# Optimization experiments

Hardware: AMD Instinct MI355X
Metric: run time of the kernel (lower is better)

## Reference

```python
import jax, jax.numpy as jnp
import numpy as np
import math

B = 200        # graphs
NPG = 512      # nodes per graph
EPG = 8192     # edges per graph (avg degree 16)
E = B * EPG
FIN = 11
H = 128


def setup_inputs() -> dict:
    key = jax.random.key(0)
    ks = jax.random.split(key, 16)
    g = jnp.arange(E, dtype=jnp.int32) // EPG  # graph id per edge
    edge_src = g * NPG + jax.random.randint(ks[0], (E,), 0, NPG, dtype=jnp.int32)
    edge_dst = g * NPG + jax.random.randint(ks[1], (E,), 0, NPG, dtype=jnp.int32)
    x = jax.random.normal(ks[2], (B * NPG, FIN), dtype=jnp.float32)

    def w(k, shape):
        return jax.random.normal(k, shape, dtype=jnp.float32) * 0.1

    return dict(
        x=x, edge_src=edge_src, edge_dst=edge_dst,
        num_graphs=B, nodes_per_graph=NPG,
        Wrel1=w(ks[3], (H, FIN)), Wroot1=w(ks[4], (H, FIN)), b1=jnp.zeros((H,), jnp.float32), pw1=w(ks[5], (H,)),
        Wrel2=w(ks[6], (H, H)), Wroot2=w(ks[7], (H, H)), b2=jnp.zeros((H,), jnp.float32), pw2=w(ks[8], (H,)),
        Wrel3=w(ks[9], (H, H)), Wroot3=w(ks[10], (H, H)), b3=jnp.zeros((H,), jnp.float32), pw3=w(ks[11], (H,)),
        Wl1=w(ks[12], (512, 256)), bl1=jnp.zeros((512,), jnp.float32),
        Wl2=w(ks[13], (64, 512)), bl2=jnp.zeros((64,), jnp.float32),
        Wl3=w(ks[14], (1, 64)), bl3=jnp.zeros((1,), jnp.float32),
    )


def graph_conv(x, src, dst, emask, Wrel, Wroot, b):
    # PyG GraphConv (aggr='add'): lin_rel(sum_j x_j) + lin_root(x)
    msg = x[src] * emask[:, None]                    # [E, F] gather + edge mask
    agg = jax.ops.segment_sum(msg, dst, num_segments=x.shape[0])
    return agg @ Wrel.T + b + x @ Wroot.T


def topk_pool(x, src, dst, emask, w, ratio, B):
    # PyG TopKPooling: score = tanh((x . w)/||w||), keep top ceil(ratio*N) per graph
    N = x.shape[0] // B
    k = int(math.ceil(ratio * N))
    score = jnp.tanh((x @ w) / jnp.linalg.norm(w))   # [B*N]
    _, idx = jax.lax.top_k(score.reshape(B, N), k)   # local indices per graph
    perm = (idx + (jnp.arange(B, dtype=idx.dtype) * N)[:, None]).reshape(-1)  # [B*k]
    xk = x[perm] * score[perm][:, None]
    # old node id -> new node id (or -1 if dropped); reindex edges, mask invalid
    newid = jnp.full((B * N,), -1, dtype=jnp.int32).at[perm].set(jnp.arange(B * k, dtype=jnp.int32))
    ns, nd = newid[src], newid[dst]
    keep = emask * (ns >= 0) * (nd >= 0)
    return xk, jnp.maximum(ns, 0), jnp.maximum(nd, 0), keep.astype(x.dtype)


def readout(x, B):
    # cat([global_max_pool, global_mean_pool]); uniform graph sizes -> reshape
    xr = x.reshape(B, -1, x.shape[-1])
    return jnp.concatenate([xr.max(axis=1), xr.mean(axis=1)], axis=-1)


def reference(x, edge_src, edge_dst, num_graphs, nodes_per_graph,
              Wrel1, Wroot1, b1, pw1, Wrel2, Wroot2, b2, pw2,
              Wrel3, Wroot3, b3, pw3, Wl1, bl1, Wl2, bl2, Wl3, bl3):
    Bg = num_graphs
    src, dst = edge_src, edge_dst
    emask = jnp.ones(src.shape, x.dtype)
    h = jax.nn.relu(graph_conv(x, src, dst, emask, Wrel1, Wroot1, b1))
    h, src, dst, emask = topk_pool(h, src, dst, emask, pw1, 0.5, Bg)
    x1 = readout(h, Bg)
    h = jax.nn.relu(graph_conv(h, src, dst, emask, Wrel2, Wroot2, b2))
    h, src, dst, emask = topk_pool(h, src, dst, emask, pw2, 0.8, Bg)
    x2 = readout(h, Bg)
    h = jax.nn.relu(graph_conv(h, src, dst, emask, Wrel3, Wroot3, b3))
    h, src, dst, emask = topk_pool(h, src, dst, emask, pw3, 0.8, Bg)
    x3 = readout(h, Bg)
    z = x1 + x2 + x3
    z = jax.nn.relu(z @ Wl1.T + bl1)   # dropout p=0.7 is identity in eval mode
    z = jax.nn.relu(z @ Wl2.T + bl2)
    return z @ Wl3.T + bl3             # [B, 1]
```

## Files before the change

kernel.cpp:

```cpp
#include <hip/hip_runtime.h>
#include <math.h>

#define BG   200
#define NPGc 512
#define EPGc 8192
#define NE   (BG*EPGc)
#define N0   (BG*NPGc)
#define FINc 11
#define Hc   128
#define K1c  256
#define K2c  205
#define K3c  164
#define N1   (BG*K1c)
#define N2   (BG*K2c)
#define N3   (BG*K3c)

typedef float f32x4 __attribute__((ext_vector_type(4)));
typedef short s16x8 __attribute__((ext_vector_type(8)));

#define PL ((size_t)N1*Hc)
#define PA ((size_t)N0*32)

__device__ inline unsigned short bf16_rne(float v){
  unsigned u = __float_as_uint(v);
  unsigned r = u + 0x7FFFu + ((u >> 16) & 1u);
  return (unsigned short)(r >> 16);
}
__device__ inline float bf16_f32(unsigned short h){
  return __uint_as_float(((unsigned)h) << 16);
}
__device__ inline void split3(float v, unsigned short& r0, unsigned short& r1,
                              unsigned short& r2){
  r0 = bf16_rne(v); float v1 = v - bf16_f32(r0);
  r1 = bf16_rne(v1); float v2 = v1 - bf16_f32(r1);
  r2 = bf16_rne(v2);
}

__device__ inline size_t flIdx(int row, int k){
  return ((size_t)(row >> 4))*2048 + (size_t)(k >> 3)*128
       + (size_t)(row & 15)*8 + (size_t)(k & 7);
}
__device__ inline size_t flIdx32(int row, int k){
  return ((size_t)(row >> 4))*512 + (size_t)(k >> 3)*128
       + (size_t)(row & 15)*8 + (size_t)(k & 7);
}

__launch_bounds__(512)
__global__ void k_front(const int* __restrict__ esrc, const int* __restrict__ edst,
                        const float* __restrict__ x,
                        const float* __restrict__ Wrel1, const float* __restrict__ Wroot1,
                        const float* __restrict__ Wrel2, const float* __restrict__ Wroot2,
                        const float* __restrict__ Wrel3, const float* __restrict__ Wroot3,
                        const float* __restrict__ Wl1, const float* __restrict__ Wl2,
                        const float* __restrict__ pw1, const float* __restrict__ pw2,
                        const float* __restrict__ pw3,
                        int* __restrict__ deg, int* __restrict__ rowptr,
                        int* __restrict__ csr, float* __restrict__ xp,
                        float* __restrict__ Wl1T, float* __restrict__ Wl2T,
                        unsigned short* __restrict__ Wsp, unsigned short* __restrict__ W1S,
                        float* __restrict__ z, float* __restrict__ norms){
  int b = blockIdx.x, t = threadIdx.x;
  if (b < BG){
    __shared__ int ed[EPGc];
    __shared__ int cnt[NPGc];
    __shared__ int sc[NPGc];
    int g = b;
    cnt[t] = 0;
    __syncthreads();
    int gb = g*EPGc;
    for (int i=t; i<EPGc; i+=512){
      int dl = edst[gb+i] & (NPGc-1);
      ed[i] = dl;
      atomicAdd(&cnt[dl], 1);
    }
    __syncthreads();
    int d = cnt[t];
    sc[t] = d;
    __syncthreads();
    for (int o=1;o<NPGc;o<<=1){
      int v = (t>=o) ? sc[t-o] : 0;
      __syncthreads();
      sc[t] += v;
      __syncthreads();
    }
    deg[g*NPGc+t]    = d;
    rowptr[g*NPGc+t] = gb + sc[t] - d;
    cnt[t] = sc[t] - d;
    __syncthreads();
    for (int i=t; i<EPGc; i+=512){
      int p = atomicAdd(&cnt[ed[i]], 1);
      csr[gb+p] = esrc[gb+i];
    }
  } else if (b < 456){
    int idx = (b-200)*512 + t;
    if (idx < 256*512){
      int f = idx >> 9, tt = idx & 511;
      Wl1T[idx] = Wl1[tt*256 + f];
    }
    if (idx < 512*64){
      int f = idx >> 6, tt = idx & 63;
      Wl2T[idx] = Wl2[tt*512 + f];
    }
    if (idx < 65536){
      int L = idx >> 15, p = (idx >> 14) & 1, ck = idx & 16383;
      int c = ck >> 7, k = ck & 127;
      const float* W = L ? (p ? Wroot3 : Wrel3) : (p ? Wroot2 : Wrel2);
      unsigned short r0, r1, r2;
      split3(W[c*128 + k], r0, r1, r2);
      unsigned short* base = Wsp + (size_t)((L*2+p)*3)*16384;
      size_t fl = flIdx(c, k);
      base[fl]          = r0;
      base[16384 + fl]  = r1;
      base[32768 + fl]  = r2;
    }
    if (idx < 4096){
      int c = idx >> 5, k = idx & 31;
      float v = (k < 11) ? Wrel1[c*11 + k] : (k < 22 ? Wroot1[c*11 + (k-11)] : 0.f);
      unsigned short r0, r1, r2;
      split3(v, r0, r1, r2);
      size_t fl = flIdx32(c, k);
      W1S[fl]        = r0;
      W1S[4096 + fl] = r1;
      W1S[8192 + fl] = r2;
    }
    if (idx < BG*256) z[idx] = 0.f;
    if (b == 455){
      int w = t >> 6, lane = t & 63;
      if (w < 3){
        const float* pw = (w==0) ? pw1 : (w==1 ? pw2 : pw3);
        float v0 = pw[lane], v1 = pw[64+lane];
        float ss = v0*v0 + v1*v1;
        for (int o=32;o>0;o>>=1) ss += __shfl_xor(ss, o);
        if (lane == 0) norms[w] = sqrtf(ss);
      }
    }
  } else {
    int idx = (b-456)*512 + t;
    int n = idx >> 4, f = idx & 15;
    xp[idx] = (f < FINc) ? x[n*FINc + f] : 0.f;
  }
}

__launch_bounds__(256, 8)
__global__ void k_agg1s(const float* __restrict__ xp, const int* __restrict__ csr,
                        const int* __restrict__ rowptr, const int* __restrict__ deg,
                        unsigned short* __restrict__ AS){
  int bid = (int)((blockIdx.x & 7)*3200 + (blockIdx.x >> 3));
  int d = bid*4 + (threadIdx.x >> 6);
  if (d >= N0) return;
  int lane = threadIdx.x & 63;
  int slot = lane >> 4, f = lane & 15;
  int rs = rowptr[d], dg = deg[d];
  float a0 = 0.f, a1 = 0.f, a2 = 0.f, a3 = 0.f;
  for (int base=0; base<dg; base+=64){
    int e = base + lane;
    int s = 0;
    if (e < dg) s = csr[rs+e];
    int cnt = min(64, dg-base);
    int sv[16];
    #pragma unroll
    for (int u=0; u<16; u++) sv[u] = __shfl(s, u*4 + slot);
    #pragma unroll
    for (int u=0; u<16; u++){
      int ei = u*4 + slot;
      float v = 0.f;
      if (ei < cnt) v = xp[(sv[u] << 4) + f];
      if      ((u & 3) == 0) a0 += v;
      else if ((u & 3) == 1) a1 += v;
      else if ((u & 3) == 2) a2 += v;
      else                   a3 += v;
    }
  }
  a0 = (a0 + a1) + (a2 + a3);
  a0 += __shfl_xor(a0, 16);
  a0 += __shfl_xor(a0, 32);
  int k0 = 2*lane, k1 = k0 + 1;
  float s0 = __shfl(a0, k0 & 15);
  float s1 = __shfl(a0, k1 & 15);
  if (lane < 16){
    float v0 = (k0 < 11) ? s0 : ((k0 < 22) ? xp[(d<<4) + k0 - 11] : 0.f);
    float v1 = (k1 < 11) ? s1 : ((k1 < 22) ? xp[(d<<4) + k1 - 11] : 0.f);
    unsigned short a_0,a_1,a_2,b_0,b_1,b_2;
    split3(v0, a_0, a_1, a_2);
    split3(v1, b_0, b_1, b_2);
    size_t fl = flIdx32(d, k0);
    *(unsigned*)&AS[fl]        = (unsigned)a_0 | ((unsigned)b_0 << 16);
    *(unsigned*)&AS[PA + fl]   = (unsigned)a_1 | ((unsigned)b_1 << 16);
    *(unsigned*)&AS[2*PA + fl] = (unsigned)a_2 | ((unsigned)b_2 << 16);
  }
}

__launch_bounds__(256)
__global__ void k_conv1m(const unsigned short* __restrict__ AS,
                         const unsigned short* __restrict__ W1S,
                         const float* __restrict__ bias, const float* __restrict__ pw,
                         const float* __restrict__ norm_p,
                         float* __restrict__ hout, float* __restrict__ score, int M){
  __shared__ float scds[64][2];
  int tid = threadIdx.x;
  int w = tid >> 6, l = tid & 63;
  int wm = w >> 1, wn = w & 1;
  int lr = l & 15, lk = l >> 4;
  int m0 = blockIdx.x * 64;

  f32x4 acc[2][4];
  #pragma unroll
  for (int mi=0;mi<2;mi++)
    #pragma unroll
    for (int ni=0;ni<4;ni++) acc[mi][ni] = (f32x4){0.f,0.f,0.f,0.f};

  s16x8 af[3][2], bf[3][4];
  #pragma unroll
  for (int mi=0; mi<2; mi++){
    int tile = (m0 + wm*32 + mi*16) >> 4;
    size_t idx = (size_t)tile*512 + (size_t)lk*128 + (size_t)lr*8;
    af[0][mi] = *(const s16x8*)&AS[idx];
    af[1][mi] = *(const s16x8*)&AS[PA + idx];
    af[2][mi] = *(const s16x8*)&AS[2*PA + idx];
  }
  #pragma unroll
  for (int ni=0; ni<4; ni++){
    int ct = wn*4 + ni;
    size_t idx = (size_t)ct*512 + (size_t)lk*128 + (size_t)lr*8;
    bf[0][ni] = *(const s16x8*)&W1S[idx];
    bf[1][ni] = *(const s16x8*)&W1S[4096 + idx];
    bf[2][ni] = *(const s16x8*)&W1S[8192 + idx];
  }
  #define TRM(sa,sb) \
    _Pragma("unroll") \
    for (int ni=0; ni<4; ni++){ \
      _Pragma("unroll") \
      for (int mi=0; mi<2; mi++){ \
        acc[mi][ni] = __builtin_amdgcn_mfma_f32_16x16x32_bf16(af[sa][mi], bf[sb][ni], acc[mi][ni], 0,0,0); \
      } \
    }
  TRM(0,0) TRM(0,1) TRM(1,0) TRM(1,1) TRM(0,2) TRM(2,0)
  #undef TRM

  float nrm = *norm_p;
  float pwv[4], biasv[4];
  #pragma unroll
  for (int ni=0;ni<4;ni++){
    int col = wn*64 + ni*16 + lr;
    pwv[ni] = pw[col]; biasv[ni] = bias[col];
  }
  #pragma unroll
  for (int mi=0; mi<2; mi++){
    #pragma unroll
    for (int reg=0; reg<4; reg++){
      int rl = wm*32 + mi*16 + lk*4 + reg;
      int row = m0 + rl;
      float hv[4]; float sc = 0.f;
      #pragma unroll
      for (int ni=0; ni<4; ni++){
        hv[ni] = fmaxf(acc[mi][ni][reg] + biasv[ni], 0.f);
        sc += hv[ni]*pwv[ni];
      }
      if (row < M){
        #pragma unroll
        for (int ni=0; ni<4; ni++)
          hout[(size_t)row*Hc + wn*64 + ni*16 + lr] = hv[ni];
      }
      sc += __shfl_xor(sc,1); sc += __shfl_xor(sc,2);
      sc += __shfl_xor(sc,4); sc += __shfl_xor(sc,8);
      if (lr == 0) scds[rl][wn] = sc;
    }
  }
  __syncthreads();
  if (tid < 64){
    int row = m0 + tid;
    if (row < M) score[row] = tanhf((scds[tid][0] + scds[tid][1]) / nrm);
  }
}

template<int N, int K, int NP2, bool DOSPLIT, bool DOMLP>
__launch_bounds__(1024, 4)
__global__ void k_topg(const float* __restrict__ score, const float* __restrict__ h,
                       int* __restrict__ newid, int* __restrict__ perm,
                       const int* __restrict__ map1In, int* __restrict__ map2Out,
                       const int* __restrict__ origPrev, int* __restrict__ origOut,
                       float* __restrict__ hp, unsigned short* __restrict__ hpS,
                       float* __restrict__ z,
                       const float* __restrict__ Wl1T, const float* __restrict__ bl1,
                       const float* __restrict__ Wl2T, const float* __restrict__ bl2,
                       const float* __restrict__ Wl3, const float* __restrict__ bl3,
                       float* __restrict__ out){
  __shared__ float sv[NP2];
  __shared__ int   si[NP2];
  __shared__ int   nid[N];
  __shared__ float2 smx2[16][64];
  __shared__ float2 ssm2[16][64];
  __shared__ float zfin[256];
  __shared__ float u1[512];
  int g = blockIdx.x, t = threadIdx.x;

  float v = -INFINITY; int ix = t;
  if (t < NP2 && t < N) v = score[g*N + t];

  for (int k=2;k<=NP2;k<<=1){
    for (int j=k>>1;j>0;j>>=1){
      if (j >= 64){
        if (t < NP2){ sv[t] = v; si[t] = ix; }
        __syncthreads();
        if (t < NP2){
          int p = t ^ j;
          float vp = sv[p]; int ip = si[p];
          bool pre = (v > vp) || (v == vp && ix < ip);
          bool up = ((t & k) == 0);
          bool lower = ((t & j) == 0);
          bool keep = lower ? (pre == up) : (pre != up);
          if (!keep){ v = vp; ix = ip; }
        }
        __syncthreads();
      } else {
        if (t < NP2){
          float vp = __shfl_xor(v, j);
          int   ip = __shfl_xor(ix, j);
          bool pre = (v > vp) || (v == vp && ix < ip);
          bool up = ((t & k) == 0);
          bool lower = ((t & j) == 0);
          bool keep = lower ? (pre == up) : (pre != up);
          if (!keep){ v = vp; ix = ip; }
        }
      }
    }
  }
  if (t < NP2){ sv[t] = v; si[t] = ix; }
  __syncthreads();

  if (t < N) nid[si[t]] = (t < K) ? t : -1;
  __syncthreads();
  if (t < N) newid[g*N + t] = (nid[t] >= 0) ? g*K + nid[t] : -1;
  if (t < K){
    int old = si[t];
    perm[g*K + t] = g*N + old;
    if (origOut) origOut[g*K + t] = origPrev[g*N + old];
  }
  if (map2Out){
    for (int o = t; o < NPGc; o += 1024){
      int m = map1In[g*NPGc + o];
      int r = (m >= 0) ? nid[m - g*N] : -1;
      map2Out[g*NPGc + o] = (r >= 0) ? g*K + r : -1;
    }
  }
  __syncthreads();

  constexpr int NB = (K + 15) / 16;
  int rg = t >> 6, j2 = t & 63;
  float2 vv[NB];
  #pragma unroll
  for (int i=0; i<NB; i++){
    int r = rg + 16*i;
    float2 val = make_float2(0.f, 0.f);
    if (r < K){
      int old = si[r];
      val = *(const float2*)&h[(size_t)(g*N + old)*Hc + 2*j2];
      float sc = sv[r];
      val.x *= sc; val.y *= sc;
    }
    vv[i] = val;
  }
  float mx = -INFINITY, my = -INFINITY, sx = 0.f, sy = 0.f;
  #pragma unroll
  for (int i=0; i<NB; i++){
    int r = rg + 16*i;
    if (r < K){
      int m = g*K + r;
      if (hp) *(float2*)&hp[(size_t)m*Hc + 2*j2] = vv[i];
      if constexpr (DOSPLIT){
        unsigned short a0,a1,a2,b0,b1,b2;
        split3(vv[i].x, a0, a1, a2);
        split3(vv[i].y, b0, b1, b2);
        size_t fl = flIdx(m, 2*j2);
        *(unsigned*)&hpS[fl]        = (unsigned)a0 | ((unsigned)b0 << 16);
        *(unsigned*)&hpS[PL + fl]   = (unsigned)a1 | ((unsigned)b1 << 16);
        *(unsigned*)&hpS[2*PL + fl] = (unsigned)a2 | ((unsigned)b2 << 16);
      }
      mx = fmaxf(mx, vv[i].x); my = fmaxf(my, vv[i].y);
      sx += vv[i].x; sy += vv[i].y;
    }
  }
  smx2[rg][j2] = make_float2(mx, my);
  ssm2[rg][j2] = make_float2(sx, sy);
  __syncthreads();
  if (t < 64){
    float2 M = smx2[0][t], S = ssm2[0][t];
    #pragma unroll
    for (int u=1; u<16; u++){
      float2 m2 = smx2[u][t], s2 = ssm2[u][t];
      M.x = fmaxf(M.x, m2.x); M.y = fmaxf(M.y, m2.y);
      S.x += s2.x; S.y += s2.y;
    }
    int c0 = 2*t, c1 = 2*t + 1;
    if constexpr (DOMLP){
      zfin[c0]       = z[g*256 + c0]       + M.x;
      zfin[c1]       = z[g*256 + c1]       + M.y;
      zfin[128 + c0] = z[g*256 + 128 + c0] + S.x / (float)K;
      zfin[128 + c1] = z[g*256 + 128 + c1] + S.y / (float)K;
    } else {
      z[g*256 + c0]       += M.x;
      z[g*256 + c1]       += M.y;
      z[g*256 + 128 + c0] += S.x / (float)K;
      z[g*256 + 128 + c1] += S.y / (float)K;
    }
  }
  if constexpr (DOMLP){
    __syncthreads();
    if (t < 512){
      float acc = bl1[t];
      #pragma unroll 8
      for (int f=0; f<256; f++) acc = fmaf(zfin[f], Wl1T[f*512 + t], acc);
      u1[t] = fmaxf(acc, 0.f);
    }
    __syncthreads();
    if (t < 64){
      float acc = bl2[t];
      #pragma unroll 8
      for (int f=0; f<512; f++) acc = fmaf(u1[f], Wl2T[f*64 + t], acc);
      float vy = fmaxf(acc, 0.f) * Wl3[t];
      for (int o=32;o>0;o>>=1) vy += __shfl_xor(vy, o);
      if (t == 0) out[g] = vy + bl3[0];
    }
  }
}

__launch_bounds__(256, 4)
__global__ void k_aggHs(const int* __restrict__ orig, const int* __restrict__ map,
                        const float* __restrict__ hp,
                        const int* __restrict__ csr, const int* __restrict__ rowptr,
                        const int* __restrict__ deg, unsigned short* __restrict__ aggS,
                        int M){
  int cpx = gridDim.x >> 3;
  int bid = (int)((blockIdx.x & 7)*cpx + (blockIdx.x >> 3));
  int m = bid*4 + (threadIdx.x>>6);
  int lane = threadIdx.x & 63;
  if (m >= M) return;
  int d = orig[m];
  int rs = rowptr[d], dg = deg[d];
  int half = lane >> 5, cl = lane & 31;
  f32x4 acc[8];
  #pragma unroll
  for (int u=0;u<8;u++) acc[u] = (f32x4){0.f,0.f,0.f,0.f};
  for (int base=0; base<dg; base+=64){
    int e = base + lane;
    int ns = -1;
    if (e < dg){ int s = csr[rs+e]; ns = map[s]; }
    int cnt = min(64, dg-base);
    for (int jj=0; jj<cnt; jj+=16){
      #pragma unroll
      for (int u=0; u<8; u++){
        int ei = jj + u*2 + half;
        int nsj = __shfl(ns, ei & 63);
        if (ei < cnt && nsj >= 0){
          acc[u] += *(const f32x4*)(hp + (size_t)nsj*Hc + cl*4);
        }
      }
    }
  }
  f32x4 s4 = ((acc[0]+acc[1]) + (acc[2]+acc[3])) + ((acc[4]+acc[5]) + (acc[6]+acc[7]));
  #pragma unroll
  for (int i=0;i<4;i++) s4[i] += __shfl_xor(s4[i], 32);
  float e0 = __shfl(s4[0], lane>>1);
  float e1 = __shfl(s4[1], lane>>1);
  float e2 = __shfl(s4[2], lane>>1);
  float e3 = __shfl(s4[3], lane>>1);
  float cx = (lane&1) ? e2 : e0;
  float cy = (lane&1) ? e3 : e1;
  unsigned short x0,x1,x2,y0,y1,y2;
  split3(cx, x0, x1, x2);
  split3(cy, y0, y1, y2);
  size_t fl = flIdx(m, 2*lane);
  *(unsigned*)&aggS[fl]        = (unsigned)x0 | ((unsigned)y0 << 16);
  *(unsigned*)&aggS[PL + fl]   = (unsigned)x1 | ((unsigned)y1 << 16);
  *(unsigned*)&aggS[2*PL + fl] = (unsigned)x2 | ((unsigned)y2 << 16);
}

__launch_bounds__(256)
__global__ void k_convH(const unsigned short* __restrict__ A0s,
                        const unsigned short* __restrict__ A1s,
                        const unsigned short* __restrict__ Wsp,
                        const float* __restrict__ bias, const float* __restrict__ pw,
                        const float* __restrict__ norm_p,
                        float* __restrict__ hout, float* __restrict__ score, int M){
  __shared__ float scds[64][2];
  int tid = threadIdx.x;
  int w = tid >> 6, l = tid & 63;
  int wm = w >> 1, wn = w & 1;
  int lr = l & 15, lk = l >> 4;
  int m0 = blockIdx.x * 64;

  f32x4 acc[2][4];
  #pragma unroll
  for (int mi=0;mi<2;mi++)
    #pragma unroll
    for (int ni=0;ni<4;ni++) acc[mi][ni] = (f32x4){0.f,0.f,0.f,0.f};

  #pragma unroll
  for (int kc=0; kc<4; kc++){
    #pragma unroll
    for (int p=0; p<2; p++){
      const unsigned short* As = p ? A1s : A0s;
      const unsigned short* Wp = Wsp + (size_t)p*3*16384;
      s16x8 af[3][2], bf[3][4];
      #pragma unroll
      for (int mi=0; mi<2; mi++){
        int tile = (m0 + wm*32 + mi*16) >> 4;
        size_t idx = (size_t)tile*2048 + (size_t)(kc*4+lk)*128 + (size_t)lr*8;
        af[0][mi] = *(const s16x8*)&As[idx];
        af[1][mi] = *(const s16x8*)&As[PL + idx];
        af[2][mi] = *(const s16x8*)&As[2*PL + idx];
      }
      #pragma unroll
      for (int ni=0; ni<4; ni++){
        int ct = wn*4 + ni;
        size_t idx = (size_t)ct*2048 + (size_t)(kc*4+lk)*128 + (size_t)lr*8;
        bf[0][ni] = *(const s16x8*)&Wp[idx];
        bf[1][ni] = *(const s16x8*)&Wp[16384 + idx];
        bf[2][ni] = *(const s16x8*)&Wp[32768 + idx];
      }
      #define TRM(sa,sb) \
        _Pragma("unroll") \
        for (int ni=0; ni<4; ni++){ \
          _Pragma("unroll") \
          for (int mi=0; mi<2; mi++){ \
            acc[mi][ni] = __builtin_amdgcn_mfma_f32_16x16x32_bf16(af[sa][mi], bf[sb][ni], acc[mi][ni], 0,0,0); \
          } \
        }
      TRM(0,0) TRM(0,1) TRM(1,0) TRM(1,1) TRM(0,2) TRM(2,0)
      #undef TRM
    }
  }

  float nrm = *norm_p;
  float pwv[4], biasv[4];
  #pragma unroll
  for (int ni=0;ni<4;ni++){
    int col = wn*64 + ni*16 + lr;
    pwv[ni] = pw[col]; biasv[ni] = bias[col];
  }
  #pragma unroll
  for (int mi=0; mi<2; mi++){
    #pragma unroll
    for (int reg=0; reg<4; reg++){
      int rl = wm*32 + mi*16 + lk*4 + reg;
      int row = m0 + rl;
      float hv[4]; float sc = 0.f;
      #pragma unroll
      for (int ni=0; ni<4; ni++){
        hv[ni] = fmaxf(acc[mi][ni][reg] + biasv[ni], 0.f);
        sc += hv[ni]*pwv[ni];
      }
      if (row < M){
        #pragma unroll
        for (int ni=0; ni<4; ni++)
          hout[(size_t)row*Hc + wn*64 + ni*16 + lr] = hv[ni];
      }
      sc += __shfl_xor(sc,1); sc += __shfl_xor(sc,2);
      sc += __shfl_xor(sc,4); sc += __shfl_xor(sc,8);
      if (lr == 0) scds[rl][wn] = sc;
    }
  }
  __syncthreads();
  if (tid < 64){
    int row = m0 + tid;
    if (row < M) score[row] = tanhf((scds[tid][0] + scds[tid][1]) / nrm);
  }
}

extern "C" void kernel_launch(void* const* d_in, const int* in_sizes, int n_in,
                              void* d_out, int out_size, void* d_ws, size_t ws_size,
                              hipStream_t stream){
  const float* x     = (const float*)d_in[0];
  const int*   esrc  = (const int*)d_in[1];
  const int*   edst  = (const int*)d_in[2];
  const float* Wrel1 = (const float*)d_in[5];
  const float* Wroot1= (const float*)d_in[6];
  const float* b1    = (const float*)d_in[7];
  const float* pw1   = (const float*)d_in[8];
  const float* Wrel2 = (const float*)d_in[9];
  const float* Wroot2= (const float*)d_in[10];
  const float* b2    = (const float*)d_in[11];
  const float* pw2   = (const float*)d_in[12];
  const float* Wrel3 = (const float*)d_in[13];
  const float* Wroot3= (const float*)d_in[14];
  const float* b3    = (const float*)d_in[15];
  const float* pw3   = (const float*)d_in[16];
  const float* Wl1   = (const float*)d_in[17];
  const float* bl1   = (const float*)d_in[18];
  const float* Wl2   = (const float*)d_in[19];
  const float* bl2   = (const float*)d_in[20];
  const float* Wl3   = (const float*)d_in[21];
  const float* bl3   = (const float*)d_in[22];
  float* out = (float*)d_out;

  char* ws = (char*)d_ws;
  size_t off = 0;
  auto alloc = [&](size_t elems)->void*{
    void* p = ws + off;
    off += ((elems*4 + 255)/256)*256;
    return p;
  };
  int*   deg    = (int*)alloc(N0);
  int*   rowptr = (int*)alloc(N0);
  int*   csr    = (int*)alloc(NE);
  int*   map1   = (int*)alloc(N0);
  int*   newid2 = (int*)alloc(N1);
  int*   map2   = (int*)alloc(N0);
  int*   perm1  = (int*)alloc(N1);
  int*   perm2  = (int*)alloc(N2);
  int*   perm3  = (int*)alloc(N3);
  int*   orig3  = (int*)alloc(N2);
  float* score1 = (float*)alloc(N0);
  float* score2 = (float*)alloc(N1);
  float* score3 = (float*)alloc(N2);
  float* xp     = (float*)alloc((size_t)N0*16);
  float* Wl1T   = (float*)alloc(256*512);
  float* Wl2T   = (float*)alloc(512*64);
  unsigned short* Wsp = (unsigned short*)alloc(98304);
  unsigned short* W1S = (unsigned short*)alloc(6144);
  float* norms  = (float*)alloc(3);
  float* bigA   = (float*)alloc((size_t)N0*Hc);
  float* hB     = (float*)alloc((size_t)N1*Hc);
  float* hpA    = (float*)alloc((size_t)N1*Hc);
  unsigned short* hpS = (unsigned short*)alloc((size_t)3*N1*Hc/2);
  float* z      = (float*)alloc(BG*256);

  float* h1   = bigA;
  unsigned short* aggS = (unsigned short*)bigA;
  unsigned short* a1S  = hpS;
  float* h2   = hB;
  float* h3   = hB;

  k_front<<<3656, 512, 0, stream>>>(esrc, edst, x,
                                    Wrel1, Wroot1, Wrel2, Wroot2, Wrel3, Wroot3,
                                    Wl1, Wl2, pw1, pw2, pw3,
                                    deg, rowptr, csr, xp,
                                    Wl1T, Wl2T, Wsp, W1S, z, norms);

  k_agg1s  <<<N0/4, 256, 0, stream>>>(xp, csr, rowptr, deg, a1S);
  k_conv1m <<<N0/64, 256, 0, stream>>>(a1S, W1S, b1, pw1, norms+0, h1, score1, N0);
  k_topg<NPGc, K1c, 512, true, false><<<BG, 1024, 0, stream>>>(
      score1, h1, map1, perm1, nullptr, nullptr, nullptr, nullptr,
      hpA, hpS, z, nullptr, nullptr, nullptr, nullptr, nullptr, nullptr, nullptr);

  k_aggHs  <<<N1/4, 256, 0, stream>>>(perm1, map1, hpA, csr, rowptr, deg, aggS, N1);
  k_convH  <<<N1/64, 256, 0, stream>>>(aggS, hpS, Wsp, b2, pw2, norms+1, h2, score2, N1);
  k_topg<K1c, K2c, 256, true, false><<<BG, 1024, 0, stream>>>(
      score2, h2, newid2, perm2, map1, map2, perm1, orig3,
      hpA, hpS, z, nullptr, nullptr, nullptr, nullptr, nullptr, nullptr, nullptr);

  k_aggHs  <<<10256, 256, 0, stream>>>(orig3, map2, hpA, csr, rowptr, deg, aggS, N2);
  k_convH  <<<(N2+63)/64, 256, 0, stream>>>(aggS, hpS, Wsp + 98304, b3, pw3, norms+2,
                                            h3, score3, N2);
  k_topg<K2c, K3c, 256, false, true><<<BG, 1024, 0, stream>>>(
      score3, h3, newid2, perm3, nullptr, nullptr, nullptr, nullptr,
      nullptr, nullptr, z, Wl1T, bl1, Wl2T, bl2, Wl3, bl3, out);
}
```

Baseline: 276.2 us.

## Split fused top-k kernel into sort, gather-readout and MLP kernels

The monolithic per-graph top-k kernel, launched with 1024 threads, is split into three kernels. A sort kernel is sized to the bitonic width, so no threads sit idle during the sort. A gather/readout kernel reads the perm and score arrays from global memory and loads two rows per iteration. A separate MLP kernel runs at the end. The aim is to cut register pressure and idle threads in the sort and raise memory-level parallelism in the gather. In exchange it adds launches and a global round-trip for the sorted scores and perm.

```diff
diff --git a/kernel.cpp b/kernel.cpp
--- a/kernel.cpp
+++ b/kernel.cpp
@@ -273,111 +273,111 @@
   }
 }
 
-template<int N, int K, int NP2, bool DOSPLIT, bool DOMLP>
-__launch_bounds__(1024, 4)
-__global__ void k_topg(const float* __restrict__ score, const float* __restrict__ h,
-                       int* __restrict__ newid, int* __restrict__ perm,
-                       const int* __restrict__ map1In, int* __restrict__ map2Out,
-                       const int* __restrict__ origPrev, int* __restrict__ origOut,
-                       float* __restrict__ hp, unsigned short* __restrict__ hpS,
-                       float* __restrict__ z,
-                       const float* __restrict__ Wl1T, const float* __restrict__ bl1,
-                       const float* __restrict__ Wl2T, const float* __restrict__ bl2,
-                       const float* __restrict__ Wl3, const float* __restrict__ bl3,
-                       float* __restrict__ out){
+template<int N, int K, int NP2>
+__launch_bounds__(NP2)
+__global__ void k_sortk(const float* __restrict__ score, int* __restrict__ newid,
+                        int* __restrict__ perm,
+                        const int* __restrict__ map1In, int* __restrict__ map2Out,
+                        const int* __restrict__ origPrev, int* __restrict__ origOut,
+                        float* __restrict__ svg){
   __shared__ float sv[NP2];
   __shared__ int   si[NP2];
   __shared__ int   nid[N];
-  __shared__ float2 smx2[16][64];
-  __shared__ float2 ssm2[16][64];
-  __shared__ float zfin[256];
-  __shared__ float u1[512];
   int g = blockIdx.x, t = threadIdx.x;
 
-  float v = -INFINITY; int ix = t;
-  if (t < NP2 && t < N) v = score[g*N + t];
+  float v = (t < N) ? score[g*N + t] : -INFINITY;
+  int ix = t;
 
   for (int k=2;k<=NP2;k<<=1){
     for (int j=k>>1;j>0;j>>=1){
       if (j >= 64){
-        if (t < NP2){ sv[t] = v; si[t] = ix; }
+        sv[t] = v; si[t] = ix;
         __syncthreads();
-        if (t < NP2){
-          int p = t ^ j;
-          float vp = sv[p]; int ip = si[p];
-          bool pre = (v > vp) || (v == vp && ix < ip);
-          bool up = ((t & k) == 0);
-          bool lower = ((t & j) == 0);
-          bool keep = lower ? (pre == up) : (pre != up);
-          if (!keep){ v = vp; ix = ip; }
-        }
+        int p = t ^ j;
+        float vp = sv[p]; int ip = si[p];
+        bool pre = (v > vp) || (v == vp && ix < ip);
+        bool up = ((t & k) == 0);
+        bool lower = ((t & j) == 0);
+        bool keep = lower ? (pre == up) : (pre != up);
+        if (!keep){ v = vp; ix = ip; }
         __syncthreads();
       } else {
-        if (t < NP2){
-          float vp = __shfl_xor(v, j);
-          int   ip = __shfl_xor(ix, j);
-          bool pre = (v > vp) || (v == vp && ix < ip);
-          bool up = ((t & k) == 0);
-          bool lower = ((t & j) == 0);
-          bool keep = lower ? (pre == up) : (pre != up);
-          if (!keep){ v = vp; ix = ip; }
-        }
-      }
-    }
-  }
-  if (t < NP2){ sv[t] = v; si[t] = ix; }
+        float vp = __shfl_xor(v, j);
+        int   ip = __shfl_xor(ix, j);
+        bool pre = (v > vp) || (v == vp && ix < ip);
+        bool up = ((t & k) == 0);
+        bool lower = ((t & j) == 0);
+        bool keep = lower ? (pre == up) : (pre != up);
+        if (!keep){ v = vp; ix = ip; }
+      }
+    }
+  }
+  sv[t] = v; si[t] = ix;
   __syncthreads();
 
   if (t < N) nid[si[t]] = (t < K) ? t : -1;
   __syncthreads();
   if (t < N) newid[g*N + t] = (nid[t] >= 0) ? g*K + nid[t] : -1;
   if (t < K){
-    int old = si[t];
-    perm[g*K + t] = g*N + old;
-    if (origOut) origOut[g*K + t] = origPrev[g*N + old];
+    perm[g*K + t] = g*N + si[t];
+    svg[g*K + t]  = sv[t];
+    if (origOut) origOut[g*K + t] = origPrev[g*N + si[t]];
   }
   if (map2Out){
-    for (int o = t; o < NPGc; o += 1024){
+    for (int o = t; o < NPGc; o += NP2){
       int m = map1In[g*NPGc + o];
       int r = (m >= 0) ? nid[m - g*N] : -1;
       map2Out[g*NPGc + o] = (r >= 0) ? g*K + r : -1;
     }
   }
-  __syncthreads();
-
-  constexpr int NB = (K + 15) / 16;
+}
+
+__launch_bounds__(1024)
+__global__ void k_gath(const float* __restrict__ h, const int* __restrict__ perm,
+                       const float* __restrict__ svg, float* __restrict__ hp,
+                       unsigned short* __restrict__ hpS, float* __restrict__ z,
+                       int K, int doSplit){
+  __shared__ float2 smx2[16][64];
+  __shared__ float2 ssm2[16][64];
+  int g = blockIdx.x, t = threadIdx.x;
   int rg = t >> 6, j2 = t & 63;
-  float2 vv[NB];
-  #pragma unroll
-  for (int i=0; i<NB; i++){
-    int r = rg + 16*i;
-    float2 val = make_float2(0.f, 0.f);
-    if (r < K){
-      int old = si[r];
-      val = *(const float2*)&h[(size_t)(g*N + old)*Hc + 2*j2];
-      float sc = sv[r];
-      val.x *= sc; val.y *= sc;
-    }
-    vv[i] = val;
-  }
   float mx = -INFINITY, my = -INFINITY, sx = 0.f, sy = 0.f;
-  #pragma unroll
-  for (int i=0; i<NB; i++){
-    int r = rg + 16*i;
-    if (r < K){
-      int m = g*K + r;
-      if (hp) *(float2*)&hp[(size_t)m*Hc + 2*j2] = vv[i];
-      if constexpr (DOSPLIT){
+  for (int r0 = rg; r0 < K; r0 += 32){
+    int r1 = r0 + 16;
+    bool has1 = (r1 < K);
+    int m0 = g*K + r0;
+    int m1 = g*K + (has1 ? r1 : r0);
+    int row0 = perm[m0];
+    int row1 = perm[m1];
+    float s0 = svg[m0];
+    float s1 = svg[m1];
+    float2 v0 = *(const float2*)&h[(size_t)row0*Hc + 2*j2];
+    float2 v1 = *(const float2*)&h[(size_t)row1*Hc + 2*j2];
+    v0.x *= s0; v0.y *= s0;
+    v1.x *= s1; v1.y *= s1;
+    if (hp) *(float2*)&hp[(size_t)m0*Hc + 2*j2] = v0;
+    if (doSplit){
+      unsigned short a0,a1,a2,b0,b1,b2;
+      split3(v0.x, a0, a1, a2);
+      split3(v0.y, b0, b1, b2);
+      size_t fl = flIdx(m0, 2*j2);
+      *(unsigned*)&hpS[fl]        = (unsigned)a0 | ((unsigned)b0 << 16);
+      *(unsigned*)&hpS[PL + fl]   = (unsigned)a1 | ((unsigned)b1 << 16);
+      *(unsigned*)&hpS[2*PL + fl] = (unsigned)a2 | ((unsigned)b2 << 16);
+    }
+    mx = fmaxf(mx, v0.x); my = fmaxf(my, v0.y); sx += v0.x; sy += v0.y;
+    if (has1){
+      if (hp) *(float2*)&hp[(size_t)m1*Hc + 2*j2] = v1;
+      if (doSplit){
         unsigned short a0,a1,a2,b0,b1,b2;
-        split3(vv[i].x, a0, a1, a2);
-        split3(vv[i].y, b0, b1, b2);
-        size_t fl = flIdx(m, 2*j2);
+        split3(v1.x, a0, a1, a2);
+        split3(v1.y, b0, b1, b2);
+        size_t fl = flIdx(m1, 2*j2);
         *(unsigned*)&hpS[fl]        = (unsigned)a0 | ((unsigned)b0 << 16);
         *(unsigned*)&hpS[PL + fl]   = (unsigned)a1 | ((unsigned)b1 << 16);
         *(unsigned*)&hpS[2*PL + fl] = (unsigned)a2 | ((unsigned)b2 << 16);
       }
-      mx = fmaxf(mx, vv[i].x); my = fmaxf(my, vv[i].y);
-      sx += vv[i].x; sy += vv[i].y;
+      mx = fmaxf(mx, v1.x); my = fmaxf(my, v1.y); sx += v1.x; sy += v1.y;
     }
   }
   smx2[rg][j2] = make_float2(mx, my);
@@ -392,35 +392,10 @@
       S.x += s2.x; S.y += s2.y;
     }
     int c0 = 2*t, c1 = 2*t + 1;
-    if constexpr (DOMLP){
-      zfin[c0]       = z[g*256 + c0]       + M.x;
-      zfin[c1]       = z[g*256 + c1]       + M.y;
-      zfin[128 + c0] = z[g*256 + 128 + c0] + S.x / (float)K;
-      zfin[128 + c1] = z[g*256 + 128 + c1] + S.y / (float)K;
-    } else {
-      z[g*256 + c0]       += M.x;
-      z[g*256 + c1]       += M.y;
-      z[g*256 + 128 + c0] += S.x / (float)K;
-      z[g*256 + 128 + c1] += S.y / (float)K;
-    }
-  }
-  if constexpr (DOMLP){
-    __syncthreads();
-    if (t < 512){
-      float acc = bl1[t];
-      #pragma unroll 8
-      for (int f=0; f<256; f++) acc = fmaf(zfin[f], Wl1T[f*512 + t], acc);
-      u1[t] = fmaxf(acc, 0.f);
-    }
-    __syncthreads();
-    if (t < 64){
-      float acc = bl2[t];
-      #pragma unroll 8
-      for (int f=0; f<512; f++) acc = fmaf(u1[f], Wl2T[f*64 + t], acc);
-      float vy = fmaxf(acc, 0.f) * Wl3[t];
-      for (int o=32;o>0;o>>=1) vy += __shfl_xor(vy, o);
-      if (t == 0) out[g] = vy + bl3[0];
-    }
+    z[g*256 + c0]       += M.x;
+    z[g*256 + c1]       += M.y;
+    z[g*256 + 128 + c0] += S.x / (float)K;
+    z[g*256 + 128 + c1] += S.y / (float)K;
   }
 }
 
@@ -564,6 +539,34 @@
   if (tid < 64){
     int row = m0 + tid;
     if (row < M) score[row] = tanhf((scds[tid][0] + scds[tid][1]) / nrm);
+  }
+}
+
+__launch_bounds__(512)
+__global__ void k_mlp(const float* __restrict__ z,
+                      const float* __restrict__ Wl1T, const float* __restrict__ bl1,
+                      const float* __restrict__ Wl2T, const float* __restrict__ bl2,
+                      const float* __restrict__ Wl3, const float* __restrict__ bl3,
+                      float* __restrict__ out){
+  __shared__ float zs[256];
+  __shared__ float u1[512];
+  int g = blockIdx.x, t = threadIdx.x;
+  if (t < 256) zs[t] = z[g*256 + t];
+  __syncthreads();
+  {
+    float acc = bl1[t];
+    #pragma unroll 8
+    for (int f=0; f<256; f++) acc = fmaf(zs[f], Wl1T[f*512 + t], acc);
+    u1[t] = fmaxf(acc, 0.f);
+  }
+  __syncthreads();
+  if (t < 64){
+    float acc = bl2[t];
+    #pragma unroll 8
+    for (int f=0; f<512; f++) acc = fmaf(u1[f], Wl2T[f*64 + t], acc);
+    float v = fmaxf(acc, 0.f) * Wl3[t];
+    for (int o=32;o>0;o>>=1) v += __shfl_xor(v, o);
+    if (t == 0) out[g] = v + bl3[0];
   }
 }
 
@@ -613,6 +616,7 @@
   float* score1 = (float*)alloc(N0);
   float* score2 = (float*)alloc(N1);
   float* score3 = (float*)alloc(N2);
+  float* svg    = (float*)alloc(N1);
   float* xp     = (float*)alloc((size_t)N0*16);
   float* Wl1T   = (float*)alloc(256*512);
   float* Wl2T   = (float*)alloc(512*64);
@@ -639,20 +643,22 @@
 
   k_agg1s  <<<N0/4, 256, 0, stream>>>(xp, csr, rowptr, deg, a1S);
   k_conv1m <<<N0/64, 256, 0, stream>>>(a1S, W1S, b1, pw1, norms+0, h1, score1, N0);
-  k_topg<NPGc, K1c, 512, true, false><<<BG, 1024, 0, stream>>>(
-      score1, h1, map1, perm1, nullptr, nullptr, nullptr, nullptr,
-      hpA, hpS, z, nullptr, nullptr, nullptr, nullptr, nullptr, nullptr, nullptr);
+  k_sortk<NPGc, K1c, 512><<<BG, 512, 0, stream>>>(score1, map1, perm1,
+                                                  nullptr, nullptr, nullptr, nullptr, svg);
+  k_gath   <<<BG, 1024, 0, stream>>>(h1, perm1, svg, hpA, hpS, z, K1c, 1);
 
   k_aggHs  <<<N1/4, 256, 0, stream>>>(perm1, map1, hpA, csr, rowptr, deg, aggS, N1);
   k_convH  <<<N1/64, 256, 0, stream>>>(aggS, hpS, Wsp, b2, pw2, norms+1, h2, score2, N1);
-  k_topg<K1c, K2c, 256, true, false><<<BG, 1024, 0, stream>>>(
-      score2, h2, newid2, perm2, map1, map2, perm1, orig3,
-      hpA, hpS, z, nullptr, nullptr, nullptr, nullptr, nullptr, nullptr, nullptr);
+  k_sortk<K1c, K2c, 256><<<BG, 256, 0, stream>>>(score2, newid2, perm2,
+                                                 map1, map2, perm1, orig3, svg);
+  k_gath   <<<BG, 1024, 0, stream>>>(h2, perm2, svg, hpA, hpS, z, K2c, 1);
 
   k_aggHs  <<<10256, 256, 0, stream>>>(orig3, map2, hpA, csr, rowptr, deg, aggS, N2);
   k_convH  <<<(N2+63)/64, 256, 0, stream>>>(aggS, hpS, Wsp + 98304, b3, pw3, norms+2,
                                             h3, score3, N2);
-  k_topg<K2c, K3c, 256, false, true><<<BG, 1024, 0, stream>>>(
-      score3, h3, newid2, perm3, nullptr, nullptr, nullptr, nullptr,
-      nullptr, nullptr, z, Wl1T, bl1, Wl2T, bl2, Wl3, bl3, out);
-}
+  k_sortk<K2c, K3c, 256><<<BG, 256, 0, stream>>>(score3, newid2, perm3,
+                                                 nullptr, nullptr, nullptr, nullptr, svg);
+  k_gath   <<<BG, 1024, 0, stream>>>(h3, perm3, svg, nullptr, hpS, z, K3c, 0);
+
+  k_mlp<<<BG, 512, 0, stream>>>(z, Wl1T, bl1, Wl2T, bl2, Wl3, bl3, out);
+}
```

Measured after the change: 283.9 us. +2.8%, slower.
